# Optimization experiments

Hardware: AMD Instinct MI355X
Metric: run time of the kernel (lower is better)

The kernel has to match this reference:

```python
import jax, jax.numpy as jnp
import numpy as np

N_NODES = 100000
N_EDGES = 3200000
N_FEAT = 512
HIDDEN = 16
N_CLASSES = 64


def setup_inputs() -> dict:
    key = jax.random.key(0)
    k1, k2, k3, k4 = jax.random.split(key, 4)
    x = jax.random.normal(k1, (N_NODES, N_FEAT), dtype=jnp.float32)
    edge_index = jax.random.randint(k2, (2, N_EDGES), 0, N_NODES, dtype=jnp.int64)
    # Glorot-ish scaling keeps log_softmax numerically tame
    W1 = jax.random.normal(k3, (N_FEAT, HIDDEN), dtype=jnp.float32) / np.sqrt(N_FEAT)
    b1 = jnp.zeros((HIDDEN,), dtype=jnp.float32)
    W2 = jax.random.normal(k4, (HIDDEN, N_CLASSES), dtype=jnp.float32) / np.sqrt(HIDDEN)
    b2 = jnp.zeros((N_CLASSES,), dtype=jnp.float32)
    return {"x": x, "edge_index": edge_index, "W1": W1, "b1": b1, "W2": W2, "b2": b2}


def _gcn_conv(h, src, dst, norm, W, b, num_nodes):
    # dense transform first (PyG GCNConv order), then normalized scatter-add
    h = h @ W                                   # [N, out]
    msg = h[src] * norm[:, None]                # gather + edge scaling [E, out]
    agg = jax.ops.segment_sum(msg, dst, num_segments=num_nodes)
    return agg + b


def reference(x, edge_index, W1, b1, W2, b2):
    N = x.shape[0]
    loop = jnp.arange(N, dtype=edge_index.dtype)
    src = jnp.concatenate([edge_index[0], loop])  # add self-loops
    dst = jnp.concatenate([edge_index[1], loop])
    deg = jax.ops.segment_sum(jnp.ones_like(src, dtype=x.dtype), dst, num_segments=N)
    dinv = jax.lax.rsqrt(jnp.maximum(deg, 1.0))
    norm = dinv[src] * dinv[dst]                  # symmetric D^-1/2 A_hat D^-1/2

    h = jax.nn.relu(_gcn_conv(x, src, dst, norm, W1, b1, N))
    # dropout: identity in eval mode (training=False)
    h = _gcn_conv(h, src, dst, norm, W2, b2, N)
    return jax.nn.log_softmax(h, axis=1)
```

## Files before the change

kernel.cpp:

```cpp
#include <hip/hip_runtime.h>

#define NNODES 100000
#define NEDGES 3200000
#define NFEAT  512
#define NHID   16
#define NCLS   64
#define NB     391
#define CAP    10240
#define EPB    4096
#define NPB    782
#define GTPB   8
#define NGB    782

typedef short bf16x8 __attribute__((ext_vector_type(8)));
typedef float f32x4  __attribute__((ext_vector_type(4)));

__device__ __forceinline__ short f2bf(float f) {
    unsigned u = __float_as_uint(f);
    return (short)((u + 0x7FFFu + ((u >> 16) & 1u)) >> 16);
}
__device__ __forceinline__ float bf2f(unsigned short u) {
    return __uint_as_float((unsigned)u << 16);
}

struct PartShared {
    unsigned hist[NB];
    unsigned scn[512];
    unsigned cursor[NB];
    unsigned delta[NB];
    unsigned staged[EPB];
    unsigned short pbkt[EPB];
};
struct GemmShared { short w1t[16][520]; };
union FusedShared { PartShared p; GemmShared g; };

__global__ __launch_bounds__(512) void k_fused1(const int* __restrict__ src,
                                                const int* __restrict__ dst,
                                                unsigned* __restrict__ gcnt,
                                                unsigned* __restrict__ part,
                                                const float* __restrict__ x,
                                                const float* __restrict__ w1,
                                                unsigned short* __restrict__ hs1) {
    __shared__ FusedShared sh;
    int t = threadIdx.x;
    if (blockIdx.x < NPB) {
        int base = blockIdx.x * EPB;
        int nblk = min(EPB, NEDGES - base);
        for (int i = t; i < NB; i += 512) sh.p.hist[i] = 0;
        __syncthreads();
        unsigned pk[8]; unsigned short bk[8];
#pragma unroll
        for (int j = 0; j < 8; ++j) {
            int o = t + j * 512;
            if (o < nblk) {
                int s = src[base + o], d = dst[base + o];
                pk[j] = (unsigned)s | ((unsigned)(d & 255) << 17);
                bk[j] = (unsigned short)(d >> 8);
                atomicAdd(&sh.p.hist[bk[j]], 1u);
            } else bk[j] = 0xFFFFu;
        }
        __syncthreads();
        sh.p.scn[t] = (t < NB) ? sh.p.hist[t] : 0u;
        __syncthreads();
#pragma unroll
        for (int off = 1; off < 512; off <<= 1) {
            unsigned a = (t >= off) ? sh.p.scn[t - off] : 0u;
            __syncthreads();
            sh.p.scn[t] += a;
            __syncthreads();
        }
        for (int i = t; i < NB; i += 512) {
            unsigned h = sh.p.hist[i];
            unsigned ex = sh.p.scn[i] - h;
            sh.p.cursor[i] = ex;
            unsigned gb = h ? atomicAdd(&gcnt[i], h) : 0u;
            sh.p.delta[i] = (unsigned)i * CAP + gb - ex;
        }
        __syncthreads();
#pragma unroll
        for (int j = 0; j < 8; ++j) {
            if (bk[j] != 0xFFFFu) {
                unsigned p = atomicAdd(&sh.p.cursor[bk[j]], 1u);
                sh.p.staged[p] = pk[j];
                sh.p.pbkt[p] = bk[j];
            }
        }
        __syncthreads();
        for (int i = t; i < nblk; i += 512) {
            unsigned b = sh.p.pbkt[i];
            unsigned d = sh.p.delta[b] + (unsigned)i;
            if (d < (b + 1u) * CAP) part[d] = sh.p.staged[i];
        }
    } else {
        for (int idx = t; idx < NFEAT * NHID; idx += 512) {
            int k = idx >> 4, n = idx & 15;
            sh.g.w1t[n][k] = f2bf(w1[idx]);
        }
        __syncthreads();
        int wave = t >> 6, lane = t & 63;
        int tile = (int)(blockIdx.x - NPB) * GTPB + wave;
        if (tile >= NNODES / 16) return;
        int m = lane & 15, q = lane >> 4;
        const float* xrow = x + (size_t)(tile * 16 + m) * NFEAT + q * 8;
        const short* wrow = &sh.g.w1t[m][q * 8];
        f32x4 acc = {0.f, 0.f, 0.f, 0.f};
#pragma unroll
        for (int kb = 0; kb < NFEAT / 32; ++kb) {
            float4 a0 = *(const float4*)(xrow + kb * 32);
            float4 a1 = *(const float4*)(xrow + kb * 32 + 4);
            bf16x8 a;
            a[0] = f2bf(a0.x); a[1] = f2bf(a0.y); a[2] = f2bf(a0.z); a[3] = f2bf(a0.w);
            a[4] = f2bf(a1.x); a[5] = f2bf(a1.y); a[6] = f2bf(a1.z); a[7] = f2bf(a1.w);
            bf16x8 b = *(const bf16x8*)(wrow + kb * 32);
            acc = __builtin_amdgcn_mfma_f32_16x16x32_bf16(a, b, acc, 0, 0, 0);
        }
        unsigned short* outp = hs1 + (size_t)(tile * 16) * NHID;
#pragma unroll
        for (int r = 0; r < 4; ++r)
            outp[(q * 4 + r) * NHID + m] = (unsigned short)f2bf(acc[r]);
    }
}

__global__ __launch_bounds__(512) void k_csr(const unsigned* __restrict__ gcnt,
                                             unsigned* __restrict__ part,
                                             unsigned* __restrict__ offs,
                                             unsigned* __restrict__ cnt,
                                             float* __restrict__ dinv) {
    __shared__ unsigned hist[256], nst[256], cursor[256];
    __shared__ unsigned staged[CAP];
    int t = threadIdx.x, b = blockIdx.x;
    unsigned cb = min(gcnt[b], (unsigned)CAP);
    unsigned* seg = part + (size_t)b * CAP;
    if (t < 256) hist[t] = 0;
    __syncthreads();
    for (unsigned i = t; i < cb; i += 512)
        atomicAdd(&hist[(seg[i] >> 17) & 255u], 1u);
    __syncthreads();
    if (t < 256) nst[t] = hist[t];
    __syncthreads();
#pragma unroll
    for (int off = 1; off < 256; off <<= 1) {
        unsigned a = (t >= off && t < 256) ? nst[t - off] : 0u;
        __syncthreads();
        if (t < 256) nst[t] += a;
        __syncthreads();
    }
    if (t < 256) {
        unsigned ex = nst[t] - hist[t];
        cursor[t] = ex;
        int node = b * 256 + t;
        if (node < NNODES) {
            offs[node] = (unsigned)b * CAP + ex;
            cnt[node] = hist[t];
            dinv[node] = rsqrtf((float)hist[t] + 1.f);
        }
    }
    __syncthreads();
    for (unsigned i = t; i < cb; i += 512) {
        unsigned p = seg[i];
        unsigned r = atomicAdd(&cursor[(p >> 17) & 255u], 1u);
        staged[r] = p & 0x1FFFFu;
    }
    __syncthreads();
    for (unsigned i = t; i < cb; i += 512)
        seg[i] = staged[i];
}

__global__ __launch_bounds__(256) void k_agg1(const unsigned* __restrict__ offs,
                                              const unsigned* __restrict__ cnt,
                                              const unsigned* __restrict__ eb,
                                              const unsigned short* __restrict__ hs1,
                                              const float* __restrict__ dinv,
                                              const float* __restrict__ b1,
                                              unsigned short* __restrict__ hs2) {
    int tid = threadIdx.x;
    int node = blockIdx.x * 4 + (tid >> 6);
    int lane = tid & 63, f = lane & 15, slot = lane >> 4;
    unsigned start = offs[node];
    int deg = (int)cnt[node];
    float di = dinv[node];
    float acc = 0.f;
    int rounds = (deg + 63) >> 6;
    int cl = deg - 1;
    for (int r = 0; r < rounds; ++r) {
        int jb = r * 64 + slot * 16;
        unsigned e[16];
#pragma unroll
        for (int u = 0; u < 16; ++u) e[u] = eb[start + min(jb + u, cl)];
        float d[16], a[16];
#pragma unroll
        for (int u = 0; u < 16; ++u) d[u] = dinv[e[u]];
#pragma unroll
        for (int u = 0; u < 16; ++u) a[u] = bf2f(hs1[(size_t)e[u] * NHID + f]);
#pragma unroll
        for (int u = 0; u < 16; ++u) acc += (jb + u < deg) ? a[u] * d[u] : 0.f;
    }
    acc += __shfl_xor(acc, 16);
    acc += __shfl_xor(acc, 32);
    float v = (acc + bf2f(hs1[(size_t)node * NHID + f]) * di) * di + b1[f];
    v = v > 0.f ? v : 0.f;
    if (slot == 0) hs2[(size_t)node * NHID + f] = (unsigned short)f2bf(v * di);
}

__global__ __launch_bounds__(256) void k_out2(const unsigned* __restrict__ offs,
                                              const unsigned* __restrict__ cnt,
                                              const unsigned* __restrict__ eb,
                                              const unsigned short* __restrict__ hs2,
                                              const float* __restrict__ dinv,
                                              const float* __restrict__ w2,
                                              const float* __restrict__ b2,
                                              float* __restrict__ out) {
    int tid = threadIdx.x;
    int node = blockIdx.x * 4 + (tid >> 6);
    int lane = tid & 63, f = lane & 15, slot = lane >> 4;
    unsigned start = offs[node];
    int deg = (int)cnt[node];
    float di = dinv[node];
    float w2c[NHID];
#pragma unroll
    for (int k = 0; k < NHID; ++k) w2c[k] = w2[k * NCLS + lane];
    float bb = b2[lane];
    float acc = 0.f;
    int rounds = (deg + 63) >> 6;
    int cl = deg - 1;
    for (int r = 0; r < rounds; ++r) {
        int jb = r * 64 + slot * 16;
        unsigned e[16];
#pragma unroll
        for (int u = 0; u < 16; ++u) e[u] = eb[start + min(jb + u, cl)];
        float a[16];
#pragma unroll
        for (int u = 0; u < 16; ++u) a[u] = bf2f(hs2[(size_t)e[u] * NHID + f]);
#pragma unroll
        for (int u = 0; u < 16; ++u) acc += (jb + u < deg) ? a[u] : 0.f;
    }
    acc += __shfl_xor(acc, 16);
    acc += __shfl_xor(acc, 32);
    float v = (acc + bf2f(hs2[(size_t)node * NHID + f])) * di;
    float logit = bb;
#pragma unroll
    for (int k = 0; k < NHID; ++k)
        logit += __shfl(v, k) * w2c[k];
    float mx = logit;
#pragma unroll
    for (int off = 32; off > 0; off >>= 1) mx = fmaxf(mx, __shfl_xor(mx, off));
    float ex = __expf(logit - mx);
    float s = ex;
#pragma unroll
    for (int off = 32; off > 0; off >>= 1) s += __shfl_xor(s, off);
    out[(size_t)node * NCLS + lane] = logit - mx - logf(s);
}

extern "C" void kernel_launch(void* const* d_in, const int* in_sizes, int n_in,
                              void* d_out, int out_size, void* d_ws, size_t ws_size,
                              hipStream_t stream) {
    const float* x  = (const float*)d_in[0];
    const int*   ei = (const int*)d_in[1];
    const float* w1 = (const float*)d_in[2];
    const float* b1 = (const float*)d_in[3];
    const float* w2 = (const float*)d_in[4];
    const float* b2 = (const float*)d_in[5];
    const int* src = ei;
    const int* dst = ei + NEDGES;

    char* ws = (char*)d_ws;
    unsigned* gcnt = (unsigned*)(ws + 0);
    unsigned* offs = (unsigned*)(ws + 2048);
    unsigned* cnt  = (unsigned*)(ws + 402048);
    float*    dinv = (float*)   (ws + 802048);
    unsigned short* hs1 = (unsigned short*)(ws + 1202048);
    unsigned short* hs2 = (unsigned short*)(ws + 4402048);
    unsigned* part = (unsigned*)(ws + 7602048);

    hipMemsetAsync(gcnt, 0, 2048, stream);
    k_fused1<<<NPB + NGB, 512, 0, stream>>>(src, dst, gcnt, part, x, w1, hs1);
    k_csr  <<<NB, 512, 0, stream>>>(gcnt, part, offs, cnt, dinv);
    k_agg1 <<<NNODES / 4, 256, 0, stream>>>(offs, cnt, part, hs1, dinv, b1, hs2);
    k_out2 <<<NNODES / 4, 256, 0, stream>>>(offs, cnt, part, hs2, dinv, w2, b2, (float*)d_out);
}
```

Measured before the change: 470.9 us.

## Fuse CSR sort with layer-1 aggregation and prescale features by dinv

Adds a small kernel that computes dinv and multiplies hs1 rows by it, which removes the per-edge dinv gather from layer-1 aggregation. The per-bucket CSR sort and the layer-1 aggregation become one kernel that reads neighbour indices from shared memory, so the separate agg1 launch and its re-read of the sorted edge list go away. The partition phase doubles edges per block, halving the number of partition blocks. The out2 gather is narrowed from 16 to 8 edges per slot per round. Only 391 blocks now run the aggregation, which may leave much of the GPU idle, and the extra bf16 rounding of the prescaled features changes numerics slightly.

```diff
diff --git a/kernel.cpp b/kernel.cpp
--- a/kernel.cpp
+++ b/kernel.cpp
@@ -7,8 +7,7 @@
 #define NCLS   64
 #define NB     391
 #define CAP    10240
-#define EPB    4096
-#define NPB    782
+#define EPB    8192
 #define GTPB   8
 #define NGB    782
 
@@ -43,14 +42,14 @@
                                                 unsigned short* __restrict__ hs1) {
     __shared__ FusedShared sh;
     int t = threadIdx.x;
-    if (blockIdx.x < NPB) {
+    if (blockIdx.x < NB) {
         int base = blockIdx.x * EPB;
         int nblk = min(EPB, NEDGES - base);
         for (int i = t; i < NB; i += 512) sh.p.hist[i] = 0;
         __syncthreads();
-        unsigned pk[8]; unsigned short bk[8];
-#pragma unroll
-        for (int j = 0; j < 8; ++j) {
+        unsigned pk[16]; unsigned short bk[16];
+#pragma unroll
+        for (int j = 0; j < 16; ++j) {
             int o = t + j * 512;
             if (o < nblk) {
                 int s = src[base + o], d = dst[base + o];
@@ -78,7 +77,7 @@
         }
         __syncthreads();
 #pragma unroll
-        for (int j = 0; j < 8; ++j) {
+        for (int j = 0; j < 16; ++j) {
             if (bk[j] != 0xFFFFu) {
                 unsigned p = atomicAdd(&sh.p.cursor[bk[j]], 1u);
                 sh.p.staged[p] = pk[j];
@@ -98,7 +97,7 @@
         }
         __syncthreads();
         int wave = t >> 6, lane = t & 63;
-        int tile = (int)(blockIdx.x - NPB) * GTPB + wave;
+        int tile = (int)(blockIdx.x - NB) * GTPB + wave;
         if (tile >= NNODES / 16) return;
         int m = lane & 15, q = lane >> 4;
         const float* xrow = x + (size_t)(tile * 16 + m) * NFEAT + q * 8;
@@ -111,8 +110,8 @@
             bf16x8 a;
             a[0] = f2bf(a0.x); a[1] = f2bf(a0.y); a[2] = f2bf(a0.z); a[3] = f2bf(a0.w);
             a[4] = f2bf(a1.x); a[5] = f2bf(a1.y); a[6] = f2bf(a1.z); a[7] = f2bf(a1.w);
-            bf16x8 b = *(const bf16x8*)(wrow + kb * 32);
-            acc = __builtin_amdgcn_mfma_f32_16x16x32_bf16(a, b, acc, 0, 0, 0);
+            bf16x8 bfr = *(const bf16x8*)(wrow + kb * 32);
+            acc = __builtin_amdgcn_mfma_f32_16x16x32_bf16(a, bfr, acc, 0, 0, 0);
         }
         unsigned short* outp = hs1 + (size_t)(tile * 16) * NHID;
 #pragma unroll
@@ -121,14 +120,49 @@
     }
 }
 
-__global__ __launch_bounds__(512) void k_csr(const unsigned* __restrict__ gcnt,
-                                             unsigned* __restrict__ part,
-                                             unsigned* __restrict__ offs,
-                                             unsigned* __restrict__ cnt,
-                                             float* __restrict__ dinv) {
-    __shared__ unsigned hist[256], nst[256], cursor[256];
+__global__ __launch_bounds__(512) void k_scale(const unsigned* __restrict__ gcnt,
+                                               const unsigned* __restrict__ part,
+                                               float* __restrict__ dinv,
+                                               unsigned short* __restrict__ hs1) {
+    __shared__ unsigned hist[256];
+    __shared__ float dl[256];
+    int t = threadIdx.x, b = blockIdx.x;
+    unsigned cb = min(gcnt[b], (unsigned)CAP);
+    const unsigned* seg = part + (size_t)b * CAP;
+    if (t < 256) hist[t] = 0;
+    __syncthreads();
+    for (unsigned i = t; i < cb; i += 512)
+        atomicAdd(&hist[(seg[i] >> 17) & 255u], 1u);
+    __syncthreads();
+    if (t < 256) {
+        dl[t] = rsqrtf((float)hist[t] + 1.f);
+        int gn = b * 256 + t;
+        if (gn < NNODES) dinv[gn] = dl[t];
+    }
+    __syncthreads();
+    for (int i = t; i < 4096; i += 512) {
+        int nd = i >> 4, ff = i & 15;
+        int gn = b * 256 + nd;
+        if (gn < NNODES) {
+            size_t ix = (size_t)gn * NHID + ff;
+            hs1[ix] = (unsigned short)f2bf(bf2f(hs1[ix]) * dl[nd]);
+        }
+    }
+}
+
+__global__ __launch_bounds__(512) void k_sortagg1(const unsigned* __restrict__ gcnt,
+                                                  unsigned* __restrict__ part,
+                                                  unsigned* __restrict__ offs,
+                                                  unsigned* __restrict__ cnt,
+                                                  const unsigned short* __restrict__ hs1,
+                                                  const float* __restrict__ b1,
+                                                  unsigned short* __restrict__ hs2) {
     __shared__ unsigned staged[CAP];
+    __shared__ unsigned hist[256], cum[256], cur[256];
+    __shared__ float dl[256];
     int t = threadIdx.x, b = blockIdx.x;
+    int lane = t & 63, wv = t >> 6;
+    int f = lane & 15, slot = lane >> 4;
     unsigned cb = min(gcnt[b], (unsigned)CAP);
     unsigned* seg = part + (size_t)b * CAP;
     if (t < 256) hist[t] = 0;
@@ -136,70 +170,60 @@
     for (unsigned i = t; i < cb; i += 512)
         atomicAdd(&hist[(seg[i] >> 17) & 255u], 1u);
     __syncthreads();
-    if (t < 256) nst[t] = hist[t];
+    if (t < 256) cum[t] = hist[t];
     __syncthreads();
 #pragma unroll
     for (int off = 1; off < 256; off <<= 1) {
-        unsigned a = (t >= off && t < 256) ? nst[t - off] : 0u;
-        __syncthreads();
-        if (t < 256) nst[t] += a;
+        unsigned a = (t >= off && t < 256) ? cum[t - off] : 0u;
+        __syncthreads();
+        if (t < 256) cum[t] += a;
         __syncthreads();
     }
     if (t < 256) {
-        unsigned ex = nst[t] - hist[t];
-        cursor[t] = ex;
+        unsigned ex = cum[t] - hist[t];
+        cur[t] = ex;
+        dl[t] = rsqrtf((float)hist[t] + 1.f);
         int node = b * 256 + t;
         if (node < NNODES) {
             offs[node] = (unsigned)b * CAP + ex;
             cnt[node] = hist[t];
-            dinv[node] = rsqrtf((float)hist[t] + 1.f);
         }
     }
     __syncthreads();
     for (unsigned i = t; i < cb; i += 512) {
         unsigned p = seg[i];
-        unsigned r = atomicAdd(&cursor[(p >> 17) & 255u], 1u);
+        unsigned r = atomicAdd(&cur[(p >> 17) & 255u], 1u);
         staged[r] = p & 0x1FFFFu;
     }
     __syncthreads();
     for (unsigned i = t; i < cb; i += 512)
         seg[i] = staged[i];
-}
-
-__global__ __launch_bounds__(256) void k_agg1(const unsigned* __restrict__ offs,
-                                              const unsigned* __restrict__ cnt,
-                                              const unsigned* __restrict__ eb,
-                                              const unsigned short* __restrict__ hs1,
-                                              const float* __restrict__ dinv,
-                                              const float* __restrict__ b1,
-                                              unsigned short* __restrict__ hs2) {
-    int tid = threadIdx.x;
-    int node = blockIdx.x * 4 + (tid >> 6);
-    int lane = tid & 63, f = lane & 15, slot = lane >> 4;
-    unsigned start = offs[node];
-    int deg = (int)cnt[node];
-    float di = dinv[node];
-    float acc = 0.f;
-    int rounds = (deg + 63) >> 6;
-    int cl = deg - 1;
-    for (int r = 0; r < rounds; ++r) {
-        int jb = r * 64 + slot * 16;
-        unsigned e[16];
-#pragma unroll
-        for (int u = 0; u < 16; ++u) e[u] = eb[start + min(jb + u, cl)];
-        float d[16], a[16];
-#pragma unroll
-        for (int u = 0; u < 16; ++u) d[u] = dinv[e[u]];
-#pragma unroll
-        for (int u = 0; u < 16; ++u) a[u] = bf2f(hs1[(size_t)e[u] * NHID + f]);
-#pragma unroll
-        for (int u = 0; u < 16; ++u) acc += (jb + u < deg) ? a[u] * d[u] : 0.f;
-    }
-    acc += __shfl_xor(acc, 16);
-    acc += __shfl_xor(acc, 32);
-    float v = (acc + bf2f(hs1[(size_t)node * NHID + f]) * di) * di + b1[f];
-    v = v > 0.f ? v : 0.f;
-    if (slot == 0) hs2[(size_t)node * NHID + f] = (unsigned short)f2bf(v * di);
+    float b1f = b1[f];
+    for (int nd = wv; nd < 256; nd += 8) {
+        int gn = b * 256 + nd;
+        if (gn >= NNODES) continue;
+        int lstart = (int)(cum[nd] - hist[nd]);
+        int deg = (int)hist[nd];
+        float di = dl[nd];
+        float acc = 0.f;
+        int rounds = (deg + 31) >> 5, cl = deg - 1;
+        for (int r = 0; r < rounds; ++r) {
+            int jb = r * 32 + slot * 8;
+            unsigned e[8];
+#pragma unroll
+            for (int u = 0; u < 8; ++u) e[u] = staged[lstart + min(jb + u, cl)];
+            float a[8];
+#pragma unroll
+            for (int u = 0; u < 8; ++u) a[u] = bf2f(hs1[(size_t)e[u] * NHID + f]);
+#pragma unroll
+            for (int u = 0; u < 8; ++u) acc += (jb + u < deg) ? a[u] : 0.f;
+        }
+        acc += __shfl_xor(acc, 16);
+        acc += __shfl_xor(acc, 32);
+        float v = (acc + bf2f(hs1[(size_t)gn * NHID + f])) * di + b1f;
+        v = v > 0.f ? v : 0.f;
+        if (slot == 0) hs2[(size_t)gn * NHID + f] = (unsigned short)f2bf(v * di);
+    }
 }
 
 __global__ __launch_bounds__(256) void k_out2(const unsigned* __restrict__ offs,
@@ -221,18 +245,18 @@
     for (int k = 0; k < NHID; ++k) w2c[k] = w2[k * NCLS + lane];
     float bb = b2[lane];
     float acc = 0.f;
-    int rounds = (deg + 63) >> 6;
+    int rounds = (deg + 31) >> 5;
     int cl = deg - 1;
     for (int r = 0; r < rounds; ++r) {
-        int jb = r * 64 + slot * 16;
-        unsigned e[16];
-#pragma unroll
-        for (int u = 0; u < 16; ++u) e[u] = eb[start + min(jb + u, cl)];
-        float a[16];
-#pragma unroll
-        for (int u = 0; u < 16; ++u) a[u] = bf2f(hs2[(size_t)e[u] * NHID + f]);
-#pragma unroll
-        for (int u = 0; u < 16; ++u) acc += (jb + u < deg) ? a[u] : 0.f;
+        int jb = r * 32 + slot * 8;
+        unsigned e[8];
+#pragma unroll
+        for (int u = 0; u < 8; ++u) e[u] = eb[start + min(jb + u, cl)];
+        float a[8];
+#pragma unroll
+        for (int u = 0; u < 8; ++u) a[u] = bf2f(hs2[(size_t)e[u] * NHID + f]);
+#pragma unroll
+        for (int u = 0; u < 8; ++u) acc += (jb + u < deg) ? a[u] : 0.f;
     }
     acc += __shfl_xor(acc, 16);
     acc += __shfl_xor(acc, 32);
@@ -273,8 +297,8 @@
     unsigned* part = (unsigned*)(ws + 7602048);
 
     hipMemsetAsync(gcnt, 0, 2048, stream);
-    k_fused1<<<NPB + NGB, 512, 0, stream>>>(src, dst, gcnt, part, x, w1, hs1);
-    k_csr  <<<NB, 512, 0, stream>>>(gcnt, part, offs, cnt, dinv);
-    k_agg1 <<<NNODES / 4, 256, 0, stream>>>(offs, cnt, part, hs1, dinv, b1, hs2);
-    k_out2 <<<NNODES / 4, 256, 0, stream>>>(offs, cnt, part, hs2, dinv, w2, b2, (float*)d_out);
-}
+    k_fused1  <<<NB + NGB, 512, 0, stream>>>(src, dst, gcnt, part, x, w1, hs1);
+    k_scale   <<<NB, 512, 0, stream>>>(gcnt, part, dinv, hs1);
+    k_sortagg1<<<NB, 512, 0, stream>>>(gcnt, part, offs, cnt, hs1, b1, hs2);
+    k_out2    <<<NNODES / 4, 256, 0, stream>>>(offs, cnt, part, hs2, dinv, w2, b2, (float*)d_out);
+}
```

Result: faster. 427.1 us (-9.3%).
